# Optimization experiments

Hardware: AMD Instinct MI355X
Metric: run time of the kernel (lower is better)

The kernel has to match this reference:

```python
import jax, jax.numpy as jnp
import numpy as np
import math

B, C, H, W = 16, 512, 32, 32
GROUPS = 32
EPS = 1e-5


def group_norm(x, w, b):
    # x: [B, C, H, W]; normalize within each of GROUPS channel groups over (C//G, H, W)
    Bx, Cx, Hx, Wx = x.shape
    xg = x.reshape(Bx, GROUPS, Cx // GROUPS, Hx, Wx)
    mean = xg.mean(axis=(2, 3, 4), keepdims=True)
    var = xg.var(axis=(2, 3, 4), keepdims=True)
    xg = (xg - mean) * jax.lax.rsqrt(var + EPS)
    xn = xg.reshape(Bx, Cx, Hx, Wx)
    return xn * w[None, :, None, None] + b[None, :, None, None]


def setup_inputs() -> dict:
    key = jax.random.key(0)
    ks = jax.random.split(key, 4)
    x = jax.random.normal(ks[0], (B, C, H, W), dtype=jnp.float32)
    gn_w = jnp.ones((C,), dtype=jnp.float32)
    gn_b = jnp.zeros((C,), dtype=jnp.float32)
    # Conv2d 1x1 weights as [out, in] matrices; PyTorch default init scale
    qkv_w = jax.random.normal(ks[1], (3 * C, C), dtype=jnp.float32) * (1.0 / math.sqrt(C))
    qkv_b = jnp.zeros((3 * C,), dtype=jnp.float32)
    out_w = jax.random.normal(ks[2], (C, C), dtype=jnp.float32) * (1.0 / math.sqrt(C))
    out_b = jnp.zeros((C,), dtype=jnp.float32)
    return {"x": x, "gn_w": gn_w, "gn_b": gn_b, "qkv_w": qkv_w,
            "qkv_b": qkv_b, "out_w": out_w, "out_b": out_b}


def reference(x, gn_w, gn_b, qkv_w, qkv_b, out_w, out_b):
    Bx, Cx, Hx, Wx = x.shape
    N = Hx * Wx
    h = group_norm(x, gn_w, gn_b)                       # [B, C, H, W]
    hf = h.reshape(Bx, Cx, N)                           # [B, C, N]
    # 1x1 conv == channel matmul
    qkv = jnp.einsum('oc,bcn->bon', qkv_w, hf) + qkv_b[None, :, None]  # [B, 3C, N]
    q, k, v = jnp.split(qkv, 3, axis=1)                 # each [B, C, N]
    q = q.transpose(0, 2, 1)                            # [B, N, C]
    v = v.transpose(0, 2, 1)                            # [B, N, C]
    scale = 1.0 / math.sqrt(Cx)
    attn = jnp.einsum('bnc,bcm->bnm', q, k) * scale     # [B, N, N]
    attn = jax.nn.softmax(attn, axis=-1)
    o = jnp.einsum('bnm,bmc->bnc', attn, v)             # [B, N, C]
    o = o.transpose(0, 2, 1)                            # [B, C, N]
    o = jnp.einsum('oc,bcn->bon', out_w, o) + out_b[None, :, None]
    return x + o.reshape(Bx, Cx, Hx, Wx)
```

## Files before the change

### kernel.cpp

```cpp
#include <hip/hip_runtime.h>

typedef unsigned short u16;
typedef short short8 __attribute__((ext_vector_type(8)));
typedef float floatx4 __attribute__((ext_vector_type(4)));
typedef u16 u16x4 __attribute__((ext_vector_type(4)));
typedef u16 u16x8 __attribute__((ext_vector_type(8)));

#define DEVI __device__ __forceinline__

DEVI u16 f2bf(float x) {
    union { float f; unsigned u; } c; c.f = x;
    unsigned u = c.u;
    u += 0x7fffu + ((u >> 16) & 1u);
    return (u16)(u >> 16);
}
DEVI float bf2f(u16 h) {
    union { unsigned u; float f; } c; c.u = ((unsigned)h) << 16;
    return c.f;
}

DEVI void gload_lds16(const void* g, void* l) {
    auto gp = (const __attribute__((address_space(1))) unsigned*)(unsigned long long)g;
    auto lp = (__attribute__((address_space(3))) unsigned*)(unsigned)(unsigned long long)l;
    __builtin_amdgcn_global_load_lds(gp, lp, 16, 0, 0);
}

__global__ __launch_bounds__(256) void gn_fused_kernel(const float* __restrict__ x,
                                                       const float* __restrict__ w,
                                                       const float* __restrict__ bb,
                                                       u16* __restrict__ h) {
    const int bg = blockIdx.x;
    const int b = bg >> 5, g = bg & 31;
    const float* xg = x + (long long)bg * 16384;
    const int n0 = threadIdx.x * 4;

    float4 xv[16];
    float s = 0.f, s2 = 0.f;
    #pragma unroll
    for (int cc = 0; cc < 16; cc++) {
        xv[cc] = *(const float4*)&xg[cc * 1024 + n0];
        s  += xv[cc].x + xv[cc].y + xv[cc].z + xv[cc].w;
        s2 += xv[cc].x*xv[cc].x + xv[cc].y*xv[cc].y + xv[cc].z*xv[cc].z + xv[cc].w*xv[cc].w;
    }
    #pragma unroll
    for (int m = 1; m < 64; m <<= 1) { s += __shfl_xor(s, m, 64); s2 += __shfl_xor(s2, m, 64); }
    __shared__ float rs[4], rq[4];
    if ((threadIdx.x & 63) == 0) { rs[threadIdx.x >> 6] = s; rq[threadIdx.x >> 6] = s2; }
    __syncthreads();
    float mean = (rs[0] + rs[1] + rs[2] + rs[3]) * (1.f / 16384.f);
    float var  = (rq[0] + rq[1] + rq[2] + rq[3]) * (1.f / 16384.f) - mean * mean;
    float rstd = rsqrtf(var + 1e-5f);

    u16x8 o[4][2];
    #pragma unroll
    for (int cc = 0; cc < 16; cc++) {
        int c = g * 16 + cc;
        float sc = w[c] * rstd;
        float sh = bb[c] - mean * sc;
        o[0][cc >> 3][cc & 7] = f2bf(xv[cc].x * sc + sh);
        o[1][cc >> 3][cc & 7] = f2bf(xv[cc].y * sc + sh);
        o[2][cc >> 3][cc & 7] = f2bf(xv[cc].z * sc + sh);
        o[3][cc >> 3][cc & 7] = f2bf(xv[cc].w * sc + sh);
    }
    u16* hb = h + ((long long)b * 1024 + n0) * 512 + g * 16;
    #pragma unroll
    for (int k = 0; k < 4; k++) {
        *(u16x8*)&hb[(long long)k * 512]     = o[k][0];
        *(u16x8*)&hb[(long long)k * 512 + 8] = o[k][1];
    }
}

__global__ __launch_bounds__(256) void wconv_kernel(const float* __restrict__ w1, u16* __restrict__ o1,
                                                    const float* __restrict__ w2, u16* __restrict__ o2) {
    int i = blockIdx.x * 256 + threadIdx.x;
    const float* src; u16* dst; int j;
    if (i < 196608) { src = w1; dst = o1; j = i; }
    else            { src = w2; dst = o2; j = i - 196608; }
    float4 v = *(const float4*)&src[j * 4];
    u16x4 p; p[0] = f2bf(v.x); p[1] = f2bf(v.y); p[2] = f2bf(v.z); p[3] = f2bf(v.w);
    *(u16x4*)&dst[j * 4] = p;
}

__global__ __launch_bounds__(256) void lreduce_kernel(const float* __restrict__ ps,
                                                      float* __restrict__ invl) {
    int i = blockIdx.x * 256 + threadIdx.x;
    int z = i >> 10, n = i & 1023;
    float l = 0.f;
    #pragma unroll
    for (int kb = 0; kb < 8; kb++) l += ps[((z * 8 + kb) << 10) + n];
    invl[i] = 1.f / l;
}

template <int MODE, int NX, int NY, bool STATS>
__global__ __launch_bounds__(256, 3)
void gemm_bt_kernel(const u16* __restrict__ A, const u16* __restrict__ Bt,
                    void* __restrict__ C0,
                    const float* __restrict__ bias, const float* __restrict__ res,
                    float* __restrict__ aux,
                    float scale, int lda, int ldb, int ldc,
                    long long sA, long long sB, long long sC, long long sR, int K) {
    int bx, by, bz;
    if (NX > 0) {
        const int lid  = blockIdx.x;
        const int xcd  = lid & 7;
        const int slot = lid >> 3;
        const int per  = NX * NY;
        const int j    = slot / per;
        const int w    = slot - j * per;
        bz = xcd + 8 * j;
        bx = w % NX;
        by = w / NX;
    } else {
        bx = blockIdx.x; by = blockIdx.y; bz = blockIdx.z;
    }
    const int t    = threadIdx.x;
    const int lane = t & 63;
    const int wave = t >> 6;
    const int m0   = by * 128;
    const int n0   = bx * 128;
    A  += (long long)bz * sA;
    Bt += (long long)bz * sB;

    __shared__ __align__(16) u16 smem[16384];
    u16* As = smem;
    u16* Bs = smem + 8192;

    const int wm = wave >> 1, wn = wave & 1;
    const int quad = lane >> 4, lrow = lane & 15;

    floatx4 acc[4][4];
    #pragma unroll
    for (int i = 0; i < 4; i++)
        #pragma unroll
        for (int j = 0; j < 4; j++)
            #pragma unroll
            for (int r = 0; r < 4; r++) acc[i][j][r] = 0.f;

    const int rowA = t >> 2;
    const int kch  = (t & 3) * 8;
    const u16* Ag = A  + (long long)(m0 + rowA) * lda + kch;
    const u16* Bg = Bt + (long long)(n0 + rowA) * ldb + kch;
    u16* Al = &As[t * 8];
    u16* Bl = &Bs[t * 8];
    const long long a64 = (long long)64 * lda;
    const long long b64 = (long long)64 * ldb;

    for (int k0 = 0; k0 < K; k0 += 64) {
        gload_lds16(Ag + k0,            Al);
        gload_lds16(Ag + k0 + a64,      Al + 2048);
        gload_lds16(Ag + k0 + 32,       Al + 4096);
        gload_lds16(Ag + k0 + 32 + a64, Al + 6144);
        gload_lds16(Bg + k0,            Bl);
        gload_lds16(Bg + k0 + b64,      Bl + 2048);
        gload_lds16(Bg + k0 + 32,       Bl + 4096);
        gload_lds16(Bg + k0 + 32 + b64, Bl + 6144);
        __syncthreads();
        #pragma unroll
        for (int kk = 0; kk < 2; kk++) {
            short8 af[4], bfr[4];
            #pragma unroll
            for (int i = 0; i < 4; i++)
                af[i] = *(const short8*)&As[kk*4096 + (wm*64 + i*16 + lrow)*32 + quad*8];
            #pragma unroll
            for (int j = 0; j < 4; j++)
                bfr[j] = *(const short8*)&Bs[kk*4096 + (wn*64 + j*16 + lrow)*32 + quad*8];
            #pragma unroll
            for (int i = 0; i < 4; i++)
                #pragma unroll
                for (int j = 0; j < 4; j++)
                    acc[i][j] = __builtin_amdgcn_mfma_f32_16x16x32_bf16(af[i], bfr[j], acc[i][j], 0, 0, 0);
        }
        __syncthreads();
    }

    const int ST = 136;

    if (MODE == 1) {
        #pragma unroll
        for (int p = 0; p < 4; p++) {
            if (p) __syncthreads();
            if (wm == (p >> 1)) {
                #pragma unroll
                for (int ii = 0; ii < 2; ii++) {
                    const int i = (p & 1) * 2 + ii;
                    const int row = ii * 16 + quad * 4;
                    #pragma unroll
                    for (int j = 0; j < 4; j++) {
                        const int cB = wn * 64 + j * 16 + lrow;
                        #pragma unroll
                        for (int r = 0; r < 4; r++) {
                            float v = acc[i][j][r] * scale;
                            if (STATS) v = __expf(v);
                            smem[(row + r) * ST + cB] = f2bf(v);
                        }
                    }
                }
            }
            __syncthreads();
            const int rr = t >> 3, cc = (t & 7) * 16;
            u16x8 a0 = *(u16x8*)&smem[rr * ST + cc];
            u16x8 a1 = *(u16x8*)&smem[rr * ST + cc + 8];
            u16* Cp = (u16*)C0 + (long long)bz * sC + (long long)(m0 + p * 32 + rr) * ldc + n0 + cc;
            *(u16x8*)Cp = a0;
            *(u16x8*)(Cp + 8) = a1;
            if (STATS) {
                float ls = 0.f;
                #pragma unroll
                for (int e = 0; e < 8; e++)
                    ls += bf2f(a0[e]) + bf2f(a1[e]);
                #pragma unroll
                for (int m2 = 1; m2 < 8; m2 <<= 1) ls += __shfl_xor(ls, m2, 8);
                if ((t & 7) == 0)
                    aux[((long long)(bz * 8 + bx)) * 1024 + m0 + p * 32 + rr] = ls;
            }
        }
    } else if (MODE == 2) {
        #pragma unroll
        for (int p = 0; p < 4; p++) {
            if (p) __syncthreads();
            if (wn == (p >> 1)) {
                #pragma unroll
                for (int jj = 0; jj < 2; jj++) {
                    const int j = (p & 1) * 2 + jj;
                    const int row = jj * 16 + lrow;
                    #pragma unroll
                    for (int i = 0; i < 4; i++) {
                        const int mmL = wm * 64 + i * 16 + quad * 4;
                        u16x4 pk;
                        #pragma unroll
                        for (int r = 0; r < 4; r++)
                            pk[r] = f2bf(acc[i][j][r] + bias[m0 + mmL + r]);
                        *(u16x4*)&smem[row * ST + mmL] = pk;
                    }
                }
            }
            __syncthreads();
            const int rr = t >> 3, cc = (t & 7) * 16;
            u16x8 a0 = *(u16x8*)&smem[rr * ST + cc];
            u16x8 a1 = *(u16x8*)&smem[rr * ST + cc + 8];
            u16* Cp = (u16*)C0 + (long long)(n0 + p * 32 + rr) * ldc + m0 + cc;
            *(u16x8*)Cp = a0;
            *(u16x8*)(Cp + 8) = a1;
        }
    } else {
        float* smf = (float*)smem;
        const int SF = 132;
        float* C = (float*)C0 + (long long)bz * sC;
        const float* rz = res + (long long)bz * sR;
        const float* il = aux + (long long)bz * 1024;
        #pragma unroll
        for (int p = 0; p < 8; p++) {
            if (p) __syncthreads();
            if (wm == (p >> 2)) {
                const int i = p & 3;
                #pragma unroll
                for (int j = 0; j < 4; j++) {
                    const int cB = wn * 64 + j * 16 + lrow;
                    #pragma unroll
                    for (int r = 0; r < 4; r++)
                        smf[(quad * 4 + r) * SF + cB] = acc[i][j][r];
                }
            }
            __syncthreads();
            const int rr = t >> 4, cc = (t & 15) * 8;
            const float bsv = bias[m0 + p * 16 + rr];
            float4 il0 = *(const float4*)&il[n0 + cc];
            float4 il1 = *(const float4*)&il[n0 + cc + 4];
            const long long gro = (long long)(m0 + p * 16 + rr) * ldc + n0 + cc;
            float4 rv0 = *(const float4*)&rz[gro];
            float4 rv1 = *(const float4*)&rz[gro + 4];
            float4 ov0, ov1;
            ov0.x = smf[rr*SF + cc + 0] * il0.x + bsv + rv0.x;
            ov0.y = smf[rr*SF + cc + 1] * il0.y + bsv + rv0.y;
            ov0.z = smf[rr*SF + cc + 2] * il0.z + bsv + rv0.z;
            ov0.w = smf[rr*SF + cc + 3] * il0.w + bsv + rv0.w;
            ov1.x = smf[rr*SF + cc + 4] * il1.x + bsv + rv1.x;
            ov1.y = smf[rr*SF + cc + 5] * il1.y + bsv + rv1.y;
            ov1.z = smf[rr*SF + cc + 6] * il1.z + bsv + rv1.z;
            ov1.w = smf[rr*SF + cc + 7] * il1.w + bsv + rv1.w;
            *(float4*)&C[gro]     = ov0;
            *(float4*)&C[gro + 4] = ov1;
        }
    }
}

extern "C" void kernel_launch(void* const* d_in, const int* in_sizes, int n_in,
                              void* d_out, int out_size, void* d_ws, size_t ws_size,
                              hipStream_t stream) {
    (void)in_sizes; (void)n_in; (void)out_size; (void)ws_size;
    const float* x     = (const float*)d_in[0];
    const float* gn_w  = (const float*)d_in[1];
    const float* gn_b  = (const float*)d_in[2];
    const float* qkv_w = (const float*)d_in[3];
    const float* qkv_b = (const float*)d_in[4];
    const float* out_w = (const float*)d_in[5];
    const float* out_b = (const float*)d_in[6];
    float* out = (float*)d_out;

    char* ws = (char*)d_ws;
    u16*  h_t   = (u16*)ws;  ws += (size_t)16*1024*512*2;
    u16*  qkv_t = (u16*)ws;  ws += (size_t)16*1024*1536*2;
    u16*  vprm  = (u16*)ws;  ws += (size_t)512*16384*2;
    u16*  E     = (u16*)ws;  ws += (size_t)16*1024*1024*2;
    u16*  wq    = (u16*)ws;  ws += (size_t)1536*512*2;
    u16*  wo    = (u16*)ws;  ws += (size_t)512*512*2;
    float* psum = (float*)ws; ws += (size_t)16*8*1024*4;
    float* invl = (float*)ws; ws += (size_t)16*1024*4;

    wconv_kernel<<<1024, 256, 0, stream>>>(qkv_w, wq, out_w, wo);
    gn_fused_kernel<<<512, 256, 0, stream>>>(x, gn_w, gn_b, h_t);

    gemm_bt_kernel<2, 0, 0, false><<<dim3(128, 12, 1), 256, 0, stream>>>(
        wq, h_t, qkv_t, qkv_b, nullptr, nullptr, 1.0f,
        512, 512, 1536, 0, 0, 0, 0, 512);

    gemm_bt_kernel<1, 0, 0, false><<<dim3(128, 4, 1), 256, 0, stream>>>(
        wo, qkv_t + 1024, vprm, nullptr, nullptr, nullptr, 1.0f,
        512, 1536, 16384, 0, 0, 0, 0, 512);

    gemm_bt_kernel<1, 8, 8, true><<<1024, 256, 0, stream>>>(
        qkv_t, qkv_t + 512, E, nullptr, nullptr, psum, 0.044194173824159216f,
        1536, 1536, 1024,
        (long long)1024*1536, (long long)1024*1536, (long long)1024*1024, 0, 512);

    lreduce_kernel<<<64, 256, 0, stream>>>(psum, invl);

    gemm_bt_kernel<3, 8, 4, false><<<512, 256, 0, stream>>>(
        vprm, E, out, out_b, x, invl, 1.0f,
        16384, 1024, 1024,
        1024, (long long)1024*1024, (long long)512*1024, (long long)512*1024, 1024);
}
```

Baseline: 209.8 us.

## Replace QK^T and V-projection GEMMs with 256x256-tile pipelined 512-thread kernel

Adds a new GEMM kernel with 256x256 output tiles, 8 waves per block, swizzled LDS and a four-phase double-buffered pipeline. Direct-to-LDS global loads are interleaved with MFMA work under explicit vmcnt waits and priority bumps. It replaces the 128-tile kernel for the V-projection and for the exp(QK^T) stage. The row-sum partials drop from 8 to 4 per row, so lreduce now sums 4 entries. Larger tiles cut global and LDS traffic per FLOP, at the cost of lower occupancy, far fewer blocks (128 and 256) across the CUs, and heavier register pressure.

```diff
diff --git a/kernel.cpp b/kernel.cpp
--- a/kernel.cpp
+++ b/kernel.cpp
@@ -87,8 +87,158 @@
     int z = i >> 10, n = i & 1023;
     float l = 0.f;
     #pragma unroll
-    for (int kb = 0; kb < 8; kb++) l += ps[((z * 8 + kb) << 10) + n];
+    for (int kb = 0; kb < 4; kb++) l += ps[((z * 4 + kb) << 10) + n];
     invl[i] = 1.f / l;
+}
+
+#define VMCNT(N) do { asm volatile("s_waitcnt vmcnt(" #N ")" ::: "memory"); \
+                      __builtin_amdgcn_sched_barrier(0); } while (0)
+
+template <bool EXPSTATS, bool AFFINE>
+__global__ __launch_bounds__(512, 2)
+void gemm256_kernel(const u16* __restrict__ A, const u16* __restrict__ Bt,
+                    u16* __restrict__ C, float* __restrict__ aux,
+                    float scale, int lda, int ldb, int ldc,
+                    long long sA, long long sB, long long sC, int K) {
+    int bx, by, bz;
+    if (AFFINE) {
+        const int lid = blockIdx.x;
+        const int slot = lid >> 3;
+        bz = (lid & 7) + 8 * (slot >> 4);
+        const int w = slot & 15;
+        bx = w & 3; by = w >> 2;
+    } else { bx = blockIdx.x; by = blockIdx.y; bz = 0; }
+
+    const int t    = threadIdx.x;
+    const int lane = t & 63;
+    const int wave = t >> 6;
+    const int wm   = wave >> 2;
+    const int wn   = wave & 3;
+    const int quad = lane >> 4, lrow = lane & 15;
+    const int m0 = by * 256, n0 = bx * 256;
+
+    __shared__ __align__(16) u16 smem[65536];
+
+    const int NT = K >> 6;
+
+    floatx4 acc[8][4];
+    #pragma unroll
+    for (int i = 0; i < 8; i++)
+        #pragma unroll
+        for (int j = 0; j < 4; j++)
+            #pragma unroll
+            for (int r = 0; r < 4; r++) acc[i][j][r] = 0.f;
+
+    const int srow = t >> 3;
+    const int koff = ((t & 7) * 8) ^ (((t >> 5) & 1) << 4);
+    const u16* Ab = A  + (long long)bz * sA + (long long)(m0 + srow) * lda + koff;
+    const u16* Bb = Bt + (long long)bz * sB + (long long)(n0 + srow) * ldb + koff;
+
+#define STGA(BUF, HALF, KT) do { \
+    const u16* gs_ = Ab + (long long)((HALF) * 128) * lda + (KT) * 64; \
+    gload_lds16(gs_,                          smem + ((BUF)*2 + (HALF)) * 8192 + t * 8); \
+    gload_lds16(gs_ + (long long)64 * lda,    smem + ((BUF)*2 + (HALF)) * 8192 + 4096 + t * 8); \
+} while (0)
+#define STGB(BUF, HALF, KT) do { \
+    const u16* gs_ = Bb + (long long)((HALF) * 128) * ldb + (KT) * 64; \
+    gload_lds16(gs_,                          smem + 32768 + ((BUF)*2 + (HALF)) * 8192 + t * 8); \
+    gload_lds16(gs_ + (long long)64 * ldb,    smem + 32768 + ((BUF)*2 + (HALF)) * 8192 + 4096 + t * 8); \
+} while (0)
+
+    const int swz  = ((lrow >> 2) & 1) << 4;
+    const int arow = wm * 64 + lrow;
+    const int brow = wn * 32 + lrow;
+#define AIDX(BUF, QA, i, kk) (((BUF)*2 + (QA)) * 8192 + ((((arow + (i)*16) << 6) + (kk)*32 + (quad << 3)) ^ swz))
+#define BIDX(BUF, QB, j, kk) (32768 + ((BUF)*2 + (QB)) * 8192 + ((((brow + (j)*16) << 6) + (kk)*32 + (quad << 3)) ^ swz))
+
+#define PHASE(BUF, QA, QB, STG_STMT) do { \
+    short8 paf[4][2], pbf[2][2]; \
+    _Pragma("unroll") for (int i = 0; i < 4; ++i) { \
+        paf[i][0] = *(const short8*)&smem[AIDX(BUF, QA, i, 0)]; \
+        paf[i][1] = *(const short8*)&smem[AIDX(BUF, QA, i, 1)]; } \
+    _Pragma("unroll") for (int j = 0; j < 2; ++j) { \
+        pbf[j][0] = *(const short8*)&smem[BIDX(BUF, QB, j, 0)]; \
+        pbf[j][1] = *(const short8*)&smem[BIDX(BUF, QB, j, 1)]; } \
+    STG_STMT; \
+    __builtin_amdgcn_s_barrier(); \
+    __builtin_amdgcn_s_setprio(1); \
+    _Pragma("unroll") for (int i = 0; i < 4; ++i) \
+        _Pragma("unroll") for (int j = 0; j < 2; ++j) { \
+            acc[(QA)*4 + i][(QB)*2 + j] = __builtin_amdgcn_mfma_f32_16x16x32_bf16( \
+                paf[i][0], pbf[j][0], acc[(QA)*4 + i][(QB)*2 + j], 0, 0, 0); \
+            acc[(QA)*4 + i][(QB)*2 + j] = __builtin_amdgcn_mfma_f32_16x16x32_bf16( \
+                paf[i][1], pbf[j][1], acc[(QA)*4 + i][(QB)*2 + j], 0, 0, 0); } \
+    __builtin_amdgcn_s_setprio(0); \
+    __builtin_amdgcn_s_barrier(); \
+} while (0)
+
+    STGA(0, 0, 0); STGA(0, 1, 0); STGB(0, 0, 0); STGB(0, 1, 0);
+    STGA(1, 0, 1); STGB(1, 0, 1);
+    asm volatile("s_waitcnt vmcnt(0)" ::: "memory");
+    __builtin_amdgcn_s_barrier();
+
+    for (int tau = 0; tau < NT - 1; ++tau) {
+        const int buf = tau & 1, nbuf = buf ^ 1;
+        const bool s2 = tau < NT - 2;
+        VMCNT(8); PHASE(buf, 0, 0, { STGA(nbuf, 1, tau + 1); });
+        VMCNT(8); PHASE(buf, 1, 0, { STGB(nbuf, 1, tau + 1); });
+        VMCNT(8); PHASE(buf, 0, 1, { if (s2) STGB(buf, 0, tau + 2); });
+                  PHASE(buf, 1, 1, { if (s2) STGA(buf, 0, tau + 2); });
+    }
+    {
+        const int buf = (NT - 1) & 1;
+        VMCNT(4); PHASE(buf, 0, 0, {});
+        VMCNT(2); PHASE(buf, 1, 0, {});
+        VMCNT(0); PHASE(buf, 0, 1, {});
+                  PHASE(buf, 1, 1, {});
+    }
+
+    const int ST2 = 272;
+    const int erow = t >> 3;
+    const int ec0  = (t & 7) * 32;
+    #pragma unroll
+    for (int s = 0; s < 4; ++s) {
+        if (s) __syncthreads();
+        if (wm == (s & 1)) {
+            const int qa = s >> 1;
+            #pragma unroll
+            for (int i = 0; i < 4; ++i)
+                #pragma unroll
+                for (int cf = 0; cf < 4; ++cf) {
+                    const int col = (cf >> 1) * 128 + wn * 32 + (cf & 1) * 16 + lrow;
+                    #pragma unroll
+                    for (int r = 0; r < 4; ++r) {
+                        float v = acc[qa * 4 + i][cf][r] * scale;
+                        if (EXPSTATS) v = __expf(v);
+                        smem[(i * 16 + quad * 4 + r) * ST2 + col] = f2bf(v);
+                    }
+                }
+        }
+        __syncthreads();
+        u16x8 y[4];
+        #pragma unroll
+        for (int kq = 0; kq < 4; ++kq) y[kq] = *(u16x8*)&smem[erow * ST2 + ec0 + kq * 8];
+        u16* Cp = C + (long long)bz * sC + (long long)(m0 + s * 64 + erow) * ldc + n0 + ec0;
+        #pragma unroll
+        for (int kq = 0; kq < 4; ++kq) *(u16x8*)(Cp + kq * 8) = y[kq];
+        if (EXPSTATS) {
+            float ls = 0.f;
+            #pragma unroll
+            for (int kq = 0; kq < 4; ++kq)
+                #pragma unroll
+                for (int e = 0; e < 8; ++e) ls += bf2f(y[kq][e]);
+            ls += __shfl_xor(ls, 1, 64);
+            ls += __shfl_xor(ls, 2, 64);
+            ls += __shfl_xor(ls, 4, 64);
+            if ((t & 7) == 0)
+                aux[((long long)(bz * 4 + bx)) * 1024 + m0 + s * 64 + erow] = ls;
+        }
+    }
+#undef STGA
+#undef STGB
+#undef AIDX
+#undef BIDX
+#undef PHASE
 }
 
 template <int MODE, int NX, int NY, bool STATS>
@@ -175,46 +325,7 @@
 
     const int ST = 136;
 
-    if (MODE == 1) {
-        #pragma unroll
-        for (int p = 0; p < 4; p++) {
-            if (p) __syncthreads();
-            if (wm == (p >> 1)) {
-                #pragma unroll
-                for (int ii = 0; ii < 2; ii++) {
-                    const int i = (p & 1) * 2 + ii;
-                    const int row = ii * 16 + quad * 4;
-                    #pragma unroll
-                    for (int j = 0; j < 4; j++) {
-                        const int cB = wn * 64 + j * 16 + lrow;
-                        #pragma unroll
-                        for (int r = 0; r < 4; r++) {
-                            float v = acc[i][j][r] * scale;
-                            if (STATS) v = __expf(v);
-                            smem[(row + r) * ST + cB] = f2bf(v);
-                        }
-                    }
-                }
-            }
-            __syncthreads();
-            const int rr = t >> 3, cc = (t & 7) * 16;
-            u16x8 a0 = *(u16x8*)&smem[rr * ST + cc];
-            u16x8 a1 = *(u16x8*)&smem[rr * ST + cc + 8];
-            u16* Cp = (u16*)C0 + (long long)bz * sC + (long long)(m0 + p * 32 + rr) * ldc + n0 + cc;
-            *(u16x8*)Cp = a0;
-            *(u16x8*)(Cp + 8) = a1;
-            if (STATS) {
-                float ls = 0.f;
-                #pragma unroll
-                for (int e = 0; e < 8; e++)
-                    ls += bf2f(a0[e]) + bf2f(a1[e]);
-                #pragma unroll
-                for (int m2 = 1; m2 < 8; m2 <<= 1) ls += __shfl_xor(ls, m2, 8);
-                if ((t & 7) == 0)
-                    aux[((long long)(bz * 8 + bx)) * 1024 + m0 + p * 32 + rr] = ls;
-            }
-        }
-    } else if (MODE == 2) {
+    if (MODE == 2) {
         #pragma unroll
         for (int p = 0; p < 4; p++) {
             if (p) __syncthreads();
@@ -314,14 +425,14 @@
         wq, h_t, qkv_t, qkv_b, nullptr, nullptr, 1.0f,
         512, 512, 1536, 0, 0, 0, 0, 512);
 
-    gemm_bt_kernel<1, 0, 0, false><<<dim3(128, 4, 1), 256, 0, stream>>>(
-        wo, qkv_t + 1024, vprm, nullptr, nullptr, nullptr, 1.0f,
-        512, 1536, 16384, 0, 0, 0, 0, 512);
-
-    gemm_bt_kernel<1, 8, 8, true><<<1024, 256, 0, stream>>>(
-        qkv_t, qkv_t + 512, E, nullptr, nullptr, psum, 0.044194173824159216f,
+    gemm256_kernel<false, false><<<dim3(64, 2, 1), 512, 0, stream>>>(
+        wo, qkv_t + 1024, vprm, nullptr, 1.0f,
+        512, 1536, 16384, 0, 0, 0, 512);
+
+    gemm256_kernel<true, true><<<256, 512, 0, stream>>>(
+        qkv_t, qkv_t + 512, E, psum, 0.044194173824159216f,
         1536, 1536, 1024,
-        (long long)1024*1536, (long long)1024*1536, (long long)1024*1024, 0, 512);
+        (long long)1024*1536, (long long)1024*1536, (long long)1024*1024, 512);
 
     lreduce_kernel<<<64, 256, 0, stream>>>(psum, invl);
 
```

After: 229.7 us. 1.09x slower.
